# Performance work log

Hardware: AMD Instinct MI355X
Metric: run time of the kernel (lower is better)

Reference implementation:

```python
import jax, jax.numpy as jnp
import numpy as np

N = 300000; E = N - 1; A = 150000; D = 64; H = 128; T = 512
NEG_SLOPE = 0.2


def _gatv2(h, src, dst, Wl, bl, Wr, br, att, bias):
    # PyG GATv2Conv, heads=1, add_self_loops=False
    xl = h @ Wl + bl            # source transform [N,H]
    xr = h @ Wr + br            # target transform [N,H]
    e = xl[src] + xr[dst]       # [E,H]
    a = jax.nn.leaky_relu(e, NEG_SLOPE) @ att   # [E]
    amax = jax.ops.segment_max(a, dst, num_segments=N)
    ex = jnp.exp(a - amax[dst])
    denom = jax.ops.segment_sum(ex, dst, num_segments=N)
    alpha = ex / (denom[dst] + 1e-16)
    out = jax.ops.segment_sum(alpha[:, None] * xl[src], dst, num_segments=N)
    return out + bias


def setup_inputs() -> dict:
    ks = jax.random.split(jax.random.key(0), 32)
    s = 0.02
    inp = {
        'x': jax.random.normal(ks[0], (N, D), jnp.float32),
        'edge_index': jax.random.randint(ks[1], (2, E), 0, N),
        'focal_seq': jax.random.normal(ks[2], (1, D), jnp.float32),
        'child_idx': jax.random.randint(ks[3], (A,), 0, N),
        'parent_idx': jax.random.randint(ks[4], (A,), 0, N + 1) - 1,  # include -1 (no parent)
        'time_idx': jax.random.randint(ks[5], (A,), 0, T),
        'W_embed': jax.random.normal(ks[6], (D, H)) * s, 'b_embed': jnp.zeros((H,)),
        'bu_Wl': jax.random.normal(ks[7], (H, H)) * s, 'bu_bl': jnp.zeros((H,)),
        'bu_Wr': jax.random.normal(ks[8], (H, H)) * s, 'bu_br': jnp.zeros((H,)),
        'bu_att': jax.random.normal(ks[9], (H,)) * s, 'bu_bias': jnp.zeros((H,)),
        'td_Wl': jax.random.normal(ks[10], (H, H)) * s, 'td_bl': jnp.zeros((H,)),
        'td_Wr': jax.random.normal(ks[11], (H, H)) * s, 'td_br': jnp.zeros((H,)),
        'td_att': jax.random.normal(ks[12], (H,)) * s, 'td_bias': jnp.zeros((H,)),
        'time_table': jax.random.normal(ks[13], (T, H)) * s,
        'W_comb': jax.random.normal(ks[14], (2 * H, H)) * s, 'b_comb': jnp.zeros((H,)),
        'W_a1': jax.random.normal(ks[15], (3 * H, H)) * s, 'b_a1': jnp.zeros((H,)),
        'W_a2': jax.random.normal(ks[16], (H, 1)) * s, 'b_a2': jnp.zeros((1,)),
        'W_seq': jax.random.normal(ks[17], (D, H)) * s, 'b_seq': jnp.zeros((H,)),
    }
    return inp


def reference(x, edge_index, focal_seq, child_idx, parent_idx, time_idx,
              W_embed, b_embed,
              bu_Wl, bu_bl, bu_Wr, bu_br, bu_att, bu_bias,
              td_Wl, td_bl, td_Wr, td_br, td_att, td_bias,
              time_table, W_comb, b_comb, W_a1, b_a1, W_a2, b_a2,
              W_seq, b_seq):
    h = x @ W_embed + b_embed                       # [N,H]
    # bottom-up pass: edge_index flipped -> src=row1, dst=row0
    h_bu = _gatv2(h, edge_index[1], edge_index[0], bu_Wl, bu_bl, bu_Wr, bu_br, bu_att, bu_bias)
    h = h + jax.nn.relu(h_bu)
    # top-down pass: src=row0, dst=row1
    h_td = _gatv2(h, edge_index[0], edge_index[1], td_Wl, td_bl, td_Wr, td_br, td_att, td_bias)
    h = h + jax.nn.relu(h_td)
    context = focal_seq @ W_seq + b_seq             # [1,H]
    h_child = h[child_idx]                          # [A,H]
    h_parent = jnp.where((parent_idx == -1)[:, None], 0.0, h[parent_idx])
    branch = jnp.concatenate([h_child, h_parent], axis=-1) @ W_comb + b_comb  # [A,H]
    t_emb = time_table[time_idx]                    # [A,H]
    combined = jnp.concatenate([branch, t_emb, jnp.broadcast_to(context, (branch.shape[0], context.shape[1]))], axis=-1)  # [A,3H]
    logits = jax.nn.relu(combined @ W_a1 + b_a1) @ W_a2 + b_a2  # [A,1]
    return logits
```

## Files before the change

kernel.cpp:

```cpp
#include <hip/hip_runtime.h>
#include <hip/hip_bf16.h>

#define NN 300000
#define EE 299999
#define AA 150000
#define DD 64
#define HH 128
#define TT 512
#define SCAN_NB ((NN + 1023) / 1024)

typedef unsigned short u16;
typedef unsigned int u32;
typedef __attribute__((ext_vector_type(8))) short short8;
typedef __attribute__((ext_vector_type(4))) float f32x4;

__device__ __forceinline__ float bfb(u16 u) { return __uint_as_float(((u32)u) << 16); }
__device__ __forceinline__ u16 f2b(float f) {
    u32 u = __float_as_uint(f);
    u32 r = (u + 0x7FFFu + ((u >> 16) & 1u)) >> 16;
    return (u16)r;
}
__device__ __forceinline__ uint4 load8(const u16* p) { return *(const uint4*)p; }
__device__ __forceinline__ uint4 load8(const float* p) {
    float4 f1 = *(const float4*)p;
    float4 f2 = *(const float4*)(p + 4);
    union { ushort s[8]; uint4 v; } u;
    u.s[0] = f2b(f1.x); u.s[1] = f2b(f1.y); u.s[2] = f2b(f1.z); u.s[3] = f2b(f1.w);
    u.s[4] = f2b(f2.x); u.s[5] = f2b(f2.y); u.s[6] = f2b(f2.z); u.s[7] = f2b(f2.w);
    return u.v;
}
__device__ __forceinline__ void unpack8(uint4 v, float* f) {
    u32 w0 = v.x, w1 = v.y, w2 = v.z, w3 = v.w;
    f[0] = bfb((u16)w0); f[1] = bfb((u16)(w0 >> 16));
    f[2] = bfb((u16)w1); f[3] = bfb((u16)(w1 >> 16));
    f[4] = bfb((u16)w2); f[5] = bfb((u16)(w2 >> 16));
    f[6] = bfb((u16)w3); f[7] = bfb((u16)(w3 >> 16));
}
__device__ __forceinline__ int swo(int row, int kblock) {
    return row * 64 + ((kblock ^ (row & 7)) * 8);
}
__device__ __forceinline__ int swo2(int row, int kblock) {
    return row * 128 + (((kblock & 8) | ((kblock & 7) ^ (row & 7))) * 8);
}
__device__ __forceinline__ void gl_lds16(const u16* src, u16* ldsbase) {
    __builtin_amdgcn_global_load_lds((const __attribute__((address_space(1))) u32*)src,
                                     (__attribute__((address_space(3))) u32*)ldsbase, 16, 0, 0);
}

__global__ __launch_bounds__(256) void k_wtrans(const float* w0, const float* w1,
                                                const float* w2, const float* w3,
                                                const float* w4, const float* w5,
                                                const float* w6, const float* w7,
                                                u16* __restrict__ wt) {
    int widx = blockIdx.x >> 3, part = blockIdx.x & 7;
    const float* W; int K = 128;
    switch (widx) {
        case 0: W = w0; break; case 1: W = w1; break;
        case 2: W = w2; break; case 3: W = w3; break;
        case 4: W = w4; break; case 5: W = w5; break;
        case 6: W = w6; break; default: W = w7; K = 64; break;
    }
    u16* dst = wt + widx * 16384;
    int total = K * 128;
    int lo = part * 2048, hi = lo + 2048;
    if (hi > total) hi = total;
    for (int idx = lo + threadIdx.x; idx < hi; idx += 256) {
        int k = idx >> 7, n = idx & 127;
        dst[n * K + k] = f2b(W[k * 128 + n]);
    }
}

__global__ void k_ctx_c1(const float* __restrict__ focal, const float* __restrict__ Wseq,
                         const float* __restrict__ bseq, const float* __restrict__ Wa1c,
                         const float* __restrict__ ba1, float* __restrict__ c1) {
    __shared__ float cs[HH];
    int t = threadIdx.x;
    float acc = bseq[t];
    for (int d = 0; d < DD; ++d) acc = fmaf(focal[d], Wseq[d * HH + t], acc);
    cs[t] = acc;
    __syncthreads();
    float a2 = ba1[t];
    for (int k = 0; k < HH; ++k) a2 = fmaf(cs[k], Wa1c[k * HH + t], a2);
    c1[t] = a2;
}

__global__ void k_tproj(const float* __restrict__ tt, const float* __restrict__ Wa1m,
                        float* __restrict__ tproj) {
    int ti = blockIdx.x, t = threadIdx.x;
    float acc = 0.f;
    for (int k = 0; k < HH; ++k)
        acc = fmaf(tt[ti * HH + k], Wa1m[k * HH + t], acc);
    tproj[(size_t)ti * HH + t] = acc;
}

__global__ void k_hist(const int* __restrict__ dst, int* __restrict__ counts) {
    int e = blockIdx.x * 256 + threadIdx.x;
    if (e < EE) atomicAdd(&counts[dst[e]], 1);
}

__global__ __launch_bounds__(256) void k_scan_block(const int* __restrict__ in,
                                                    int* __restrict__ out,
                                                    int* __restrict__ bsum, int n) {
    __shared__ int sh[256];
    int b = blockIdx.x, t = threadIdx.x;
    int base = b * 1024 + t * 4;
    int v0 = (base + 0 < n) ? in[base + 0] : 0;
    int v1 = (base + 1 < n) ? in[base + 1] : 0;
    int v2 = (base + 2 < n) ? in[base + 2] : 0;
    int v3 = (base + 3 < n) ? in[base + 3] : 0;
    int tsum = v0 + v1 + v2 + v3;
    sh[t] = tsum;
    __syncthreads();
    for (int d = 1; d < 256; d <<= 1) {
        int x = (t >= d) ? sh[t - d] : 0;
        __syncthreads();
        sh[t] += x;
        __syncthreads();
    }
    int excl = sh[t] - tsum;
    if (t == 255) bsum[b] = sh[255];
    if (base + 0 < n) out[base + 0] = excl;
    if (base + 1 < n) out[base + 1] = excl + v0;
    if (base + 2 < n) out[base + 2] = excl + v0 + v1;
    if (base + 3 < n) out[base + 3] = excl + v0 + v1 + v2;
}

__global__ __launch_bounds__(256) void k_scan_top(int* __restrict__ data, int n) {
    __shared__ int sh[256];
    int t = threadIdx.x;
    int base = t * 4;
    int v0 = (base + 0 < n) ? data[base + 0] : 0;
    int v1 = (base + 1 < n) ? data[base + 1] : 0;
    int v2 = (base + 2 < n) ? data[base + 2] : 0;
    int v3 = (base + 3 < n) ? data[base + 3] : 0;
    int tsum = v0 + v1 + v2 + v3;
    sh[t] = tsum;
    __syncthreads();
    for (int d = 1; d < 256; d <<= 1) {
        int x = (t >= d) ? sh[t - d] : 0;
        __syncthreads();
        sh[t] += x;
        __syncthreads();
    }
    int excl = sh[t] - tsum;
    if (base + 0 < n) data[base + 0] = excl;
    if (base + 1 < n) data[base + 1] = excl + v0;
    if (base + 2 < n) data[base + 2] = excl + v0 + v1;
    if (base + 3 < n) data[base + 3] = excl + v0 + v1 + v2;
}

__global__ void k_scan_add(int* __restrict__ out, const int* __restrict__ bsum, int n) {
    int i = blockIdx.x * 256 + threadIdx.x;
    if (i < n) out[i] += bsum[i >> 10];
}

__global__ void k_settail(int* o1, int* o2) {
    if (threadIdx.x == 0) { o1[NN] = EE; o2[NN] = EE; }
}

__global__ void k_scatter(const int* __restrict__ src, const int* __restrict__ dst,
                          int* __restrict__ cursor, int* __restrict__ elist) {
    int e = blockIdx.x * 256 + threadIdx.x;
    if (e >= EE) return;
    int pos = atomicAdd(&cursor[dst[e]], 1);
    elist[pos] = src[e];
}

template <int K, typename InT>
__global__ __launch_bounds__(256) void k_mfma_proj(const InT* __restrict__ in,
                                                   const u16* __restrict__ WT,
                                                   const float* __restrict__ bias,
                                                   u16* __restrict__ out, int nrows) {
    __shared__ u16 lds[17408];
    u16* a_lds = lds;
    u16* b_lds = lds + 8192;
    u16* clds = lds;
    const int t = threadIdx.x;
    const int tile_m = blockIdx.x * 128;
    const int wave = t >> 6, l = t & 15, quad = (t >> 4) & 3;
    const int wr = wave >> 1, wc = wave & 1;
    f32x4 acc[4][4] = {};

    for (int chunk = 0; chunk < K / 64; ++chunk) {
        const int c0 = chunk * 64;
        __syncthreads();
        for (int ci = t; ci < 1024; ci += 256) {
            int row = ci >> 3, kc = ci & 7;
            int grow = tile_m + row;
            uint4 v = make_uint4(0, 0, 0, 0);
            if (grow < nrows) v = load8(&in[(size_t)grow * K + c0 + kc * 8]);
            *(uint4*)&a_lds[swo(row, kc)] = v;
        }
        for (int ci = t; ci < 1024; ci += 256) {
            int n = ci >> 3, kc = ci & 7;
            *(uint4*)&b_lds[swo(n, kc)] = *(const uint4*)&WT[(size_t)n * K + c0 + kc * 8];
        }
        __syncthreads();
#pragma unroll
        for (int ks = 0; ks < 2; ++ks) {
            short8 af[4], bf[4];
#pragma unroll
            for (int i = 0; i < 4; ++i)
                af[i] = *(const short8*)&a_lds[swo(wr * 64 + i * 16 + l, ks * 4 + quad)];
#pragma unroll
            for (int j = 0; j < 4; ++j)
                bf[j] = *(const short8*)&b_lds[swo(wc * 64 + j * 16 + l, ks * 4 + quad)];
#pragma unroll
            for (int i = 0; i < 4; ++i)
#pragma unroll
                for (int j = 0; j < 4; ++j)
                    acc[i][j] = __builtin_amdgcn_mfma_f32_16x16x32_bf16(af[i], bf[j], acc[i][j], 0, 0, 0);
        }
    }
    __syncthreads();
#pragma unroll
    for (int j = 0; j < 4; ++j) {
        int col = wc * 64 + j * 16 + l;
        float b = bias[col];
#pragma unroll
        for (int i = 0; i < 4; ++i) {
            int rloc = wr * 64 + i * 16 + quad * 4;
#pragma unroll
            for (int r = 0; r < 4; ++r)
                clds[(rloc + r) * 136 + col] = f2b(acc[i][j][r] + b);
        }
    }
    __syncthreads();
#pragma unroll
    for (int it = 0; it < 8; ++it) {
        int idx = it * 256 + t;
        int row = idx >> 4, c16 = idx & 15;
        int grow = tile_m + row;
        if (grow < nrows)
            *(uint4*)&out[(size_t)grow * HH + c16 * 8] = *(const uint4*)&clds[row * 136 + c16 * 8];
    }
}

__global__ __launch_bounds__(512) void k_mfma_proj2(const u16* __restrict__ in,
                                                    const u16* __restrict__ WT1,
                                                    const u16* __restrict__ WT2,
                                                    const float* __restrict__ b1,
                                                    const float* __restrict__ b2,
                                                    u16* __restrict__ out1,
                                                    u16* __restrict__ out2, int nrows) {
    __shared__ u16 lds[24576];
    u16* a_lds = lds;
    u16* b1_lds = lds + 8192;
    u16* b2_lds = lds + 16384;
    u16* clds = lds;
    const int t = threadIdx.x;
    const int tile_m = blockIdx.x * 128;
    const int wave = t >> 6, l = t & 15, quad = (t >> 4) & 3;
    const int wr = wave >> 1, wc = wave & 1;
    f32x4 acc1[2][4] = {}, acc2[2][4] = {};

    for (int chunk = 0; chunk < 2; ++chunk) {
        const int c0 = chunk * 64;
        __syncthreads();
#pragma unroll
        for (int it = 0; it < 2; ++it) {
            int ci = it * 512 + t;
            int row = ci >> 3;
            int colblk = ((ci & 7) ^ (row & 7)) * 8;
            u16* wbase = lds + (ci & ~63) * 8;
            int grow = tile_m + row; if (grow >= nrows) grow = nrows - 1;
            gl_lds16(&in[(size_t)grow * HH + c0 + colblk], wbase);
            gl_lds16(&WT1[(size_t)row * HH + c0 + colblk], wbase + 8192);
            gl_lds16(&WT2[(size_t)row * HH + c0 + colblk], wbase + 16384);
        }
        __syncthreads();
#pragma unroll
        for (int ks = 0; ks < 2; ++ks) {
            short8 af[2], bf1[4], bf2[4];
#pragma unroll
            for (int i = 0; i < 2; ++i)
                af[i] = *(const short8*)&a_lds[swo(wr * 32 + i * 16 + l, ks * 4 + quad)];
#pragma unroll
            for (int j = 0; j < 4; ++j) {
                bf1[j] = *(const short8*)&b1_lds[swo(wc * 64 + j * 16 + l, ks * 4 + quad)];
                bf2[j] = *(const short8*)&b2_lds[swo(wc * 64 + j * 16 + l, ks * 4 + quad)];
            }
#pragma unroll
            for (int i = 0; i < 2; ++i)
#pragma unroll
                for (int j = 0; j < 4; ++j) {
                    acc1[i][j] = __builtin_amdgcn_mfma_f32_16x16x32_bf16(af[i], bf1[j], acc1[i][j], 0, 0, 0);
                    acc2[i][j] = __builtin_amdgcn_mfma_f32_16x16x32_bf16(af[i], bf2[j], acc2[i][j], 0, 0, 0);
                }
        }
    }
    __syncthreads();
#pragma unroll
    for (int j = 0; j < 4; ++j) {
        int col = wc * 64 + j * 16 + l;
        float b = b1[col];
#pragma unroll
        for (int i = 0; i < 2; ++i) {
            int rloc = wr * 32 + i * 16 + quad * 4;
#pragma unroll
            for (int r = 0; r < 4; ++r)
                clds[(rloc + r) * 136 + col] = f2b(acc1[i][j][r] + b);
        }
    }
    __syncthreads();
#pragma unroll
    for (int it = 0; it < 4; ++it) {
        int idx = it * 512 + t;
        int row = idx >> 4, c16 = idx & 15;
        int grow = tile_m + row;
        if (grow < nrows)
            *(uint4*)&out1[(size_t)grow * HH + c16 * 8] = *(const uint4*)&clds[row * 136 + c16 * 8];
    }
    __syncthreads();
#pragma unroll
    for (int j = 0; j < 4; ++j) {
        int col = wc * 64 + j * 16 + l;
        float b = b2[col];
#pragma unroll
        for (int i = 0; i < 2; ++i) {
            int rloc = wr * 32 + i * 16 + quad * 4;
#pragma unroll
            for (int r = 0; r < 4; ++r)
                clds[(rloc + r) * 136 + col] = f2b(acc2[i][j][r] + b);
        }
    }
    __syncthreads();
#pragma unroll
    for (int it = 0; it < 4; ++it) {
        int idx = it * 512 + t;
        int row = idx >> 4, c16 = idx & 15;
        int grow = tile_m + row;
        if (grow < nrows)
            *(uint4*)&out2[(size_t)grow * HH + c16 * 8] = *(const uint4*)&clds[row * 136 + c16 * 8];
    }
}

__global__ __launch_bounds__(256) void k_branch_logit(const u16* __restrict__ h,
                                                      const int* __restrict__ idx1,
                                                      const int* __restrict__ idx2,
                                                      const u16* __restrict__ WT1,
                                                      const u16* __restrict__ WT2,
                                                      const float* __restrict__ bias,
                                                      const int* __restrict__ time_idx,
                                                      const float* __restrict__ tproj,
                                                      const float* __restrict__ c1,
                                                      const u16* __restrict__ WTa1,
                                                      const float* __restrict__ Wa2,
                                                      const float* __restrict__ ba2,
                                                      float* __restrict__ out) {
    __shared__ u16 lds[24576];
    __shared__ float red[2][128];
    u16* a_lds = lds;
    u16* b_lds = lds + 8192;
    u16* abuf = lds;
    u16* z2 = lds + 16384;
    const int t = threadIdx.x;
    const int tile_m = blockIdx.x * 128;
    const int wave = t >> 6, l = t & 15, quad = (t >> 4) & 3;
    const int wr = wave >> 1, wc = wave & 1;
    f32x4 acc[4][4] = {};

    for (int pass = 0; pass < 2; ++pass) {
        const int* idx = pass ? idx2 : idx1;
        const u16* WT = pass ? WT2 : WT1;
        for (int chunk = 0; chunk < 2; ++chunk) {
            const int c0 = chunk * 64;
            __syncthreads();
            int gneg[4];
#pragma unroll
            for (int it = 0; it < 4; ++it) {
                int ci = it * 256 + t;
                int row = ci >> 3;
                int colblk = ((ci & 7) ^ (row & 7)) * 8;
                u16* wbase = lds + (ci & ~63) * 8;
                int item = tile_m + row; if (item >= AA) item = AA - 1;
                int g = idx[item];
                gneg[it] = (g < 0);
                if (g < 0) g = 0;
                gl_lds16(&h[(size_t)g * HH + c0 + colblk], wbase);
                gl_lds16(&WT[(size_t)row * HH + c0 + colblk], wbase + 8192);
            }
            __syncthreads();
#pragma unroll
            for (int it = 0; it < 4; ++it) {
                if (gneg[it]) {
                    int ci = it * 256 + t;
                    *(uint4*)&a_lds[ci * 8] = make_uint4(0, 0, 0, 0);
                }
            }
            __syncthreads();
#pragma unroll
            for (int ks = 0; ks < 2; ++ks) {
                short8 af[4], bf[4];
#pragma unroll
                for (int i = 0; i < 4; ++i)
                    af[i] = *(const short8*)&a_lds[swo(wr * 64 + i * 16 + l, ks * 4 + quad)];
#pragma unroll
                for (int j = 0; j < 4; ++j)
                    bf[j] = *(const short8*)&b_lds[swo(wc * 64 + j * 16 + l, ks * 4 + quad)];
#pragma unroll
                for (int i = 0; i < 4; ++i)
#pragma unroll
                    for (int j = 0; j < 4; ++j)
                        acc[i][j] = __builtin_amdgcn_mfma_f32_16x16x32_bf16(af[i], bf[j], acc[i][j], 0, 0, 0);
            }
        }
    }
    __syncthreads();
#pragma unroll
    for (int j = 0; j < 4; ++j) {
        int col = wc * 64 + j * 16 + l;
        float b = bias[col];
        int kb = col >> 3, ko = col & 7;
#pragma unroll
        for (int i = 0; i < 4; ++i) {
            int rloc = wr * 64 + i * 16 + quad * 4;
#pragma unroll
            for (int r = 0; r < 4; ++r)
                abuf[swo2(rloc + r, kb) + ko] = f2b(acc[i][j][r] + b);
        }
    }
    f32x4 accz[4][4] = {};
    for (int chunk = 0; chunk < 2; ++chunk) {
        const int c0 = chunk * 64;
        __syncthreads();
#pragma unroll
        for (int it = 0; it < 4; ++it) {
            int ci = it * 256 + t;
            int row = ci >> 3;
            int colblk = ((ci & 7) ^ (row & 7)) * 8;
            u16* wbase = z2 + (ci & ~63) * 8;
            gl_lds16(&WTa1[(size_t)row * HH + c0 + colblk], wbase);
        }
        __syncthreads();
#pragma unroll
        for (int ks = 0; ks < 2; ++ks) {
            short8 af[4], bf[4];
            int kb = chunk * 8 + ks * 4 + quad;
#pragma unroll
            for (int i = 0; i < 4; ++i)
                af[i] = *(const short8*)&abuf[swo2(wr * 64 + i * 16 + l, kb)];
#pragma unroll
            for (int j = 0; j < 4; ++j)
                bf[j] = *(const short8*)&z2[swo(wc * 64 + j * 16 + l, ks * 4 + quad)];
#pragma unroll
            for (int i = 0; i < 4; ++i)
#pragma unroll
                for (int j = 0; j < 4; ++j)
                    accz[i][j] = __builtin_amdgcn_mfma_f32_16x16x32_bf16(af[i], bf[j], accz[i][j], 0, 0, 0);
        }
    }
    float c1v[4], wa2v[4];
#pragma unroll
    for (int j = 0; j < 4; ++j) {
        int col = wc * 64 + j * 16 + l;
        c1v[j] = c1[col];
        wa2v[j] = Wa2[col];
    }
#pragma unroll
    for (int i = 0; i < 4; ++i) {
        int rbase = tile_m + wr * 64 + i * 16 + quad * 4;
#pragma unroll
        for (int r = 0; r < 4; ++r) {
            int item = rbase + r;
            int ti = (item < AA) ? time_idx[item] : 0;
            const float* tp = tproj + (size_t)ti * HH;
            float partial = 0.f;
#pragma unroll
            for (int j = 0; j < 4; ++j) {
                int col = wc * 64 + j * 16 + l;
                float z = fmaxf(accz[i][j][r] + tp[col] + c1v[j], 0.f);
                partial = fmaf(z, wa2v[j], partial);
            }
            partial += __shfl_xor(partial, 1);
            partial += __shfl_xor(partial, 2);
            partial += __shfl_xor(partial, 4);
            partial += __shfl_xor(partial, 8);
            if (l == 0) red[wc][wr * 64 + i * 16 + quad * 4 + r] = partial;
        }
    }
    __syncthreads();
    if (t < 128) {
        int item = tile_m + t;
        if (item < AA) out[item] = red[0][t] + red[1][t] + ba2[0];
    }
}

__global__ __launch_bounds__(256) void k_gat_fused(u16* __restrict__ h,
                                                   const u16* __restrict__ xl,
                                                   const u16* __restrict__ xr,
                                                   const int* __restrict__ offs,
                                                   const int* __restrict__ elist,
                                                   const float* __restrict__ att,
                                                   const float* __restrict__ bias) {
    int g = blockIdx.x * 16 + (threadIdx.x >> 4);
    int l = threadIdx.x & 15;
    float attv[8], biasv[8];
    *(float4*)&attv[0] = *(const float4*)&att[l * 8];
    *(float4*)&attv[4] = *(const float4*)&att[l * 8 + 4];
    *(float4*)&biasv[0] = *(const float4*)&bias[l * 8];
    *(float4*)&biasv[4] = *(const float4*)&bias[l * 8 + 4];
    float xrf[8];
    unpack8(*(const uint4*)&xr[(size_t)g * HH + l * 8], xrf);
    int e0 = offs[g], e1 = offs[g + 1];

    float m = -__builtin_inff(), s = 0.f;
    float acc[8] = {};
    for (int e = e0; e < e1; ++e) {
        int sidx = elist[e];
        float xf[8];
        unpack8(*(const uint4*)&xl[(size_t)sidx * HH + l * 8], xf);
        float p = 0.f;
#pragma unroll
        for (int j = 0; j < 8; ++j) {
            float v = xf[j] + xrf[j];
            v = v >= 0.f ? v : 0.2f * v;
            p = fmaf(v, attv[j], p);
        }
        p += __shfl_xor(p, 1); p += __shfl_xor(p, 2);
        p += __shfl_xor(p, 4); p += __shfl_xor(p, 8);
        float mn = fmaxf(m, p);
        float so = __expf(m - mn);
        float w = __expf(p - mn);
        s = s * so + w;
#pragma unroll
        for (int j = 0; j < 8; ++j) acc[j] = fmaf(acc[j], so, w * xf[j]);
        m = mn;
    }
    float inv = 1.f / (s + 1e-16f);

    float hf[8];
    unpack8(*(const uint4*)&h[(size_t)g * HH + l * 8], hf);
    union { ushort sh[8]; uint4 v; } o;
#pragma unroll
    for (int j = 0; j < 8; ++j) {
        hf[j] += fmaxf(fmaf(acc[j], inv, biasv[j]), 0.f);
        o.sh[j] = f2b(hf[j]);
    }
    *(uint4*)&h[(size_t)g * HH + l * 8] = o.v;
}

typedef const float* fp;

static void build_csr(const int* src, const int* dst, int* offs, int* elist,
                      int* work, int* bsum, hipStream_t stream) {
    hipMemsetAsync(work, 0, (size_t)NN * 4, stream);
    k_hist<<<(EE + 255) / 256, 256, 0, stream>>>(dst, work);
    k_scan_block<<<SCAN_NB, 256, 0, stream>>>(work, offs, bsum, NN);
    k_scan_top<<<1, 256, 0, stream>>>(bsum, SCAN_NB);
    k_scan_add<<<(NN + 255) / 256, 256, 0, stream>>>(offs, bsum, NN);
    hipMemcpyAsync(work, offs, (size_t)NN * 4, hipMemcpyDeviceToDevice, stream);
    k_scatter<<<(EE + 255) / 256, 256, 0, stream>>>(src, dst, work, elist);
}

extern "C" void kernel_launch(void* const* d_in, const int* in_sizes, int n_in,
                              void* d_out, int out_size, void* d_ws, size_t ws_size,
                              hipStream_t stream) {
    fp x                 = (fp)d_in[0];
    const int* ei        = (const int*)d_in[1];
    fp focal             = (fp)d_in[2];
    const int* child_idx = (const int*)d_in[3];
    const int* parent_idx= (const int*)d_in[4];
    const int* time_idx  = (const int*)d_in[5];
    fp W_embed = (fp)d_in[6],  b_embed = (fp)d_in[7];
    fp bu_Wl   = (fp)d_in[8],  bu_bl   = (fp)d_in[9];
    fp bu_Wr   = (fp)d_in[10], bu_br   = (fp)d_in[11];
    fp bu_att  = (fp)d_in[12], bu_bias = (fp)d_in[13];
    fp td_Wl   = (fp)d_in[14], td_bl   = (fp)d_in[15];
    fp td_Wr   = (fp)d_in[16], td_br   = (fp)d_in[17];
    fp td_att  = (fp)d_in[18], td_bias = (fp)d_in[19];
    fp time_table = (fp)d_in[20];
    fp W_comb  = (fp)d_in[21], b_comb  = (fp)d_in[22];
    fp W_a1    = (fp)d_in[23], b_a1    = (fp)d_in[24];
    fp W_a2    = (fp)d_in[25], b_a2    = (fp)d_in[26];
    fp W_seq   = (fp)d_in[27], b_seq   = (fp)d_in[28];

    const size_t NH = (size_t)NN * HH;
    u16* wt = (u16*)d_ws;
    u16* h  = wt + 8 * 16384;
    u16* xl = h + NH;
    u16* xr = xl + NH;
    float* c1v   = (float*)(xr + NH);
    float* tproj = c1v + HH;
    int* offsBU  = (int*)(tproj + (size_t)TT * HH);
    int* offsTD  = offsBU + NN + 1;
    int* elistBU = offsTD + NN + 1;
    int* elistTD = elistBU + EE;
    int* csr_work= elistTD + EE;
    int* bsum    = csr_work + NN;

    build_csr(ei + EE, ei, offsBU, elistBU, csr_work, bsum, stream);
    build_csr(ei, ei + EE, offsTD, elistTD, csr_work, bsum, stream);
    k_settail<<<1, 64, 0, stream>>>(offsBU, offsTD);

    k_wtrans<<<64, 256, 0, stream>>>(bu_Wl, bu_Wr, td_Wl, td_Wr,
                                     W_comb, W_comb + (size_t)HH * HH, W_a1, W_embed, wt);
    const u16* wt_buWl = wt + 0 * 16384;
    const u16* wt_buWr = wt + 1 * 16384;
    const u16* wt_tdWl = wt + 2 * 16384;
    const u16* wt_tdWr = wt + 3 * 16384;
    const u16* wt_combC = wt + 4 * 16384;
    const u16* wt_combP = wt + 5 * 16384;
    const u16* wt_a1   = wt + 6 * 16384;
    const u16* wt_embed = wt + 7 * 16384;

    k_ctx_c1<<<1, 128, 0, stream>>>(focal, W_seq, b_seq, W_a1 + (size_t)256 * HH, b_a1, c1v);
    k_tproj<<<TT, 128, 0, stream>>>(time_table, W_a1 + (size_t)128 * HH, tproj);

    const int NB = (NN + 127) / 128;
    k_mfma_proj<64, float><<<NB, 256, 0, stream>>>(x, wt_embed, b_embed, h, NN);

    k_mfma_proj2<<<NB, 512, 0, stream>>>(h, wt_buWl, wt_buWr, bu_bl, bu_br, xl, xr, NN);
    k_gat_fused<<<NN / 16, 256, 0, stream>>>(h, xl, xr, offsBU, elistBU, bu_att, bu_bias);

    k_mfma_proj2<<<NB, 512, 0, stream>>>(h, wt_tdWl, wt_tdWr, td_bl, td_br, xl, xr, NN);
    k_gat_fused<<<NN / 16, 256, 0, stream>>>(h, xl, xr, offsTD, elistTD, td_att, td_bias);

    k_branch_logit<<<(AA + 127) / 128, 256, 0, stream>>>(
        h, child_idx, parent_idx, wt_combC, wt_combP, b_comb,
        time_idx, tproj, c1v, wt_a1, W_a2, b_a2, (float*)d_out);
}
```

Baseline: 561.0 us.

## Build both CSRs in one pass and degree-sort nodes within tiles

Both CSR builds (bottom-up and top-down) are merged into one set of histogram, scan and scatter launches over a 2N concatenated count array, cutting the number of launches and edge-index passes in half. A new per-256-node tile counting sort orders nodes by degree (capped at 15), and the fused GAT kernel reads its node id through this permutation. Neighbouring 16-lane groups then handle nodes of similar degree, which reduces divergence across a wavefront. The cost is an extra permutation lookup and scattered h/xr accesses within each tile.

```diff
diff --git a/kernel.cpp b/kernel.cpp
--- a/kernel.cpp
+++ b/kernel.cpp
@@ -7,7 +7,7 @@
 #define DD 64
 #define HH 128
 #define TT 512
-#define SCAN_NB ((NN + 1023) / 1024)
+#define SCAN_NB2 ((2 * NN + 1023) / 1024)
 
 typedef unsigned short u16;
 typedef unsigned int u32;
@@ -93,9 +93,11 @@
     tproj[(size_t)ti * HH + t] = acc;
 }
 
-__global__ void k_hist(const int* __restrict__ dst, int* __restrict__ counts) {
+__global__ void k_hist2(const int* __restrict__ ei, int* __restrict__ counts) {
     int e = blockIdx.x * 256 + threadIdx.x;
-    if (e < EE) atomicAdd(&counts[dst[e]], 1);
+    if (e >= EE) return;
+    atomicAdd(&counts[ei[e]], 1);
+    atomicAdd(&counts[NN + ei[EE + e]], 1);
 }
 
 __global__ __launch_bounds__(256) void k_scan_block(const int* __restrict__ in,
@@ -154,16 +156,43 @@
     if (i < n) out[i] += bsum[i >> 10];
 }
 
-__global__ void k_settail(int* o1, int* o2) {
-    if (threadIdx.x == 0) { o1[NN] = EE; o2[NN] = EE; }
-}
-
-__global__ void k_scatter(const int* __restrict__ src, const int* __restrict__ dst,
-                          int* __restrict__ cursor, int* __restrict__ elist) {
+__global__ void k_settail(int* offs) {
+    if (threadIdx.x == 0) offs[2 * NN] = 2 * EE;
+}
+
+__global__ void k_scatter2(const int* __restrict__ ei, int* __restrict__ cursor,
+                           int* __restrict__ elist) {
     int e = blockIdx.x * 256 + threadIdx.x;
     if (e >= EE) return;
-    int pos = atomicAdd(&cursor[dst[e]], 1);
-    elist[pos] = src[e];
+    int r0 = ei[e], r1 = ei[EE + e];
+    int pB = atomicAdd(&cursor[r0], 1);      elist[pB] = r1;
+    int pT = atomicAdd(&cursor[NN + r1], 1); elist[pT] = r0;
+}
+
+__global__ __launch_bounds__(256) void k_tilesort(const int* __restrict__ counts,
+                                                  int* __restrict__ perm) {
+    __shared__ int cur[16];
+    int half = blockIdx.y;
+    int base = blockIdx.x * 256;
+    int t = threadIdx.x;
+    int node = base + t;
+    bool valid = node < NN;
+    int deg = 0;
+    if (valid) { deg = counts[half * NN + node]; if (deg > 15) deg = 15; }
+    if (t < 16) cur[t] = 0;
+    __syncthreads();
+    if (valid) atomicAdd(&cur[deg], 1);
+    __syncthreads();
+    if (t == 0) {
+        int run = 0;
+#pragma unroll
+        for (int b = 0; b < 16; ++b) { int c = cur[b]; cur[b] = run; run += c; }
+    }
+    __syncthreads();
+    if (valid) {
+        int pos = atomicAdd(&cur[deg], 1);
+        perm[half * NN + base + pos] = node;
+    }
 }
 
 template <int K, typename InT>
@@ -491,9 +520,10 @@
                                                    const u16* __restrict__ xr,
                                                    const int* __restrict__ offs,
                                                    const int* __restrict__ elist,
+                                                   const int* __restrict__ perm,
                                                    const float* __restrict__ att,
                                                    const float* __restrict__ bias) {
-    int g = blockIdx.x * 16 + (threadIdx.x >> 4);
+    int g = perm[blockIdx.x * 16 + (threadIdx.x >> 4)];
     int l = threadIdx.x & 15;
     float attv[8], biasv[8];
     *(float4*)&attv[0] = *(const float4*)&att[l * 8];
@@ -541,17 +571,6 @@
 }
 
 typedef const float* fp;
-
-static void build_csr(const int* src, const int* dst, int* offs, int* elist,
-                      int* work, int* bsum, hipStream_t stream) {
-    hipMemsetAsync(work, 0, (size_t)NN * 4, stream);
-    k_hist<<<(EE + 255) / 256, 256, 0, stream>>>(dst, work);
-    k_scan_block<<<SCAN_NB, 256, 0, stream>>>(work, offs, bsum, NN);
-    k_scan_top<<<1, 256, 0, stream>>>(bsum, SCAN_NB);
-    k_scan_add<<<(NN + 255) / 256, 256, 0, stream>>>(offs, bsum, NN);
-    hipMemcpyAsync(work, offs, (size_t)NN * 4, hipMemcpyDeviceToDevice, stream);
-    k_scatter<<<(EE + 255) / 256, 256, 0, stream>>>(src, dst, work, elist);
-}
 
 extern "C" void kernel_launch(void* const* d_in, const int* in_sizes, int n_in,
                               void* d_out, int out_size, void* d_ws, size_t ws_size,
@@ -582,16 +601,22 @@
     u16* xr = xl + NH;
     float* c1v   = (float*)(xr + NH);
     float* tproj = c1v + HH;
-    int* offsBU  = (int*)(tproj + (size_t)TT * HH);
-    int* offsTD  = offsBU + NN + 1;
-    int* elistBU = offsTD + NN + 1;
-    int* elistTD = elistBU + EE;
-    int* csr_work= elistTD + EE;
-    int* bsum    = csr_work + NN;
-
-    build_csr(ei + EE, ei, offsBU, elistBU, csr_work, bsum, stream);
-    build_csr(ei, ei + EE, offsTD, elistTD, csr_work, bsum, stream);
-    k_settail<<<1, 64, 0, stream>>>(offsBU, offsTD);
+    int* offs    = (int*)(tproj + (size_t)TT * HH);
+    int* elist   = offs + 2 * NN + 1;
+    int* counts  = elist + 2 * EE;
+    int* cursor  = counts + 2 * NN;
+    int* perm    = cursor + 2 * NN;
+    int* bsum    = perm + 2 * NN;
+
+    hipMemsetAsync(counts, 0, (size_t)2 * NN * 4, stream);
+    k_hist2<<<(EE + 255) / 256, 256, 0, stream>>>(ei, counts);
+    k_scan_block<<<SCAN_NB2, 256, 0, stream>>>(counts, offs, bsum, 2 * NN);
+    k_scan_top<<<1, 256, 0, stream>>>(bsum, SCAN_NB2);
+    k_scan_add<<<(2 * NN + 255) / 256, 256, 0, stream>>>(offs, bsum, 2 * NN);
+    k_settail<<<1, 64, 0, stream>>>(offs);
+    k_tilesort<<<dim3((NN + 255) / 256, 2), 256, 0, stream>>>(counts, perm);
+    hipMemcpyAsync(cursor, offs, (size_t)2 * NN * 4, hipMemcpyDeviceToDevice, stream);
+    k_scatter2<<<(EE + 255) / 256, 256, 0, stream>>>(ei, cursor, elist);
 
     k_wtrans<<<64, 256, 0, stream>>>(bu_Wl, bu_Wr, td_Wl, td_Wr,
                                      W_comb, W_comb + (size_t)HH * HH, W_a1, W_embed, wt);
@@ -611,10 +636,10 @@
     k_mfma_proj<64, float><<<NB, 256, 0, stream>>>(x, wt_embed, b_embed, h, NN);
 
     k_mfma_proj2<<<NB, 512, 0, stream>>>(h, wt_buWl, wt_buWr, bu_bl, bu_br, xl, xr, NN);
-    k_gat_fused<<<NN / 16, 256, 0, stream>>>(h, xl, xr, offsBU, elistBU, bu_att, bu_bias);
+    k_gat_fused<<<NN / 16, 256, 0, stream>>>(h, xl, xr, offs, elist, perm, bu_att, bu_bias);
 
     k_mfma_proj2<<<NB, 512, 0, stream>>>(h, wt_tdWl, wt_tdWr, td_bl, td_br, xl, xr, NN);
-    k_gat_fused<<<NN / 16, 256, 0, stream>>>(h, xl, xr, offsTD, elistTD, td_att, td_bias);
+    k_gat_fused<<<NN / 16, 256, 0, stream>>>(h, xl, xr, offs + NN, elist, perm + NN, td_att, td_bias);
 
     k_branch_logit<<<(AA + 127) / 128, 256, 0, stream>>>(
         h, child_idx, parent_idx, wt_combC, wt_combP, b_comb,
```

New measurement: 564.7 us. Within noise of the previous version (+0.6%).
